# Kernel tuning notes

Measured on AMD Instinct MI355X. Metric: run time of the kernel, lower is better.

## Reference

```python
import jax, jax.numpy as jnp
import numpy as np

B, N, D = 4, 2048, 1024
H = 8
DK = D // H            # 128, head qk dim (pre feature map)
DV = D // H            # 128, head v dim
DF = 2 * DK            # 256, hedgehog feature dim
CHUNK = 64
RMS_EPS = 1e-5


def setup_inputs() -> dict:
    key = jax.random.key(0)
    ks = jax.random.split(key, 10)
    s = D ** -0.5
    x = jax.random.normal(ks[0], (B, N, D), dtype=jnp.float32)
    Wq = jax.random.normal(ks[1], (D, D), dtype=jnp.float32) * s
    Wk = jax.random.normal(ks[2], (D, D), dtype=jnp.float32) * s
    Wv = jax.random.normal(ks[3], (D, D), dtype=jnp.float32) * s
    Wo = jax.random.normal(ks[4], (D, D), dtype=jnp.float32) * s
    eye = jnp.eye(DK, dtype=jnp.float32)
    # Hedgehog maps are initialized as identity; add small noise to exercise math
    fmq_w = eye + 0.02 * jax.random.normal(ks[5], (DK, DK), dtype=jnp.float32)
    fmq_b = 0.02 * jax.random.normal(ks[6], (DK,), dtype=jnp.float32)
    fmk_w = eye + 0.02 * jax.random.normal(ks[7], (DK, DK), dtype=jnp.float32)
    fmk_b = 0.02 * jax.random.normal(ks[8], (DK,), dtype=jnp.float32)
    rms_w = 1.0 + 0.1 * jax.random.normal(ks[9], (DV,), dtype=jnp.float32)
    return {"x": x, "Wq": Wq, "Wk": Wk, "Wv": Wv, "Wo": Wo,
            "fmq_w": fmq_w, "fmq_b": fmq_b, "fmk_w": fmk_w, "fmk_b": fmk_b,
            "rms_w": rms_w}


def _hedgehog(x, w, b):
    # x: [B,H,N,DK]; Linear then concat(exp(y), exp(-y)) -> [B,H,N,2*DK]
    y = jnp.einsum('bhnd,ed->bhne', x, w) + b
    return jnp.concatenate([jnp.exp(y), jnp.exp(-y)], axis=-1)


def _fused_chunk_linear_attn(q, k, v):
    # Causal linear attention via chunked recurrence.
    # q,k: [B,H,N,DF]; v: [B,H,N,DV]; q already scaled.
    b, h, n, df = q.shape
    dv = v.shape[-1]
    nc = n // CHUNK
    def to_chunks(t):
        d = t.shape[-1]
        return t.reshape(b, h, nc, CHUNK, d).transpose(2, 0, 1, 3, 4)  # [Nc,B,H,C,d]
    qc, kc, vc = to_chunks(q), to_chunks(k), to_chunks(v)
    mask = jnp.tril(jnp.ones((CHUNK, CHUNK), dtype=bool))

    def step(S, inp):
        qi, ki, vi = inp                                   # [B,H,C,*]
        attn = jnp.einsum('bhcd,bhed->bhce', qi, ki)       # intra-chunk scores
        attn = jnp.where(mask, attn, 0.0)                  # causal (inclusive)
        intra = jnp.einsum('bhce,bhev->bhcv', attn, vi)
        inter = jnp.einsum('bhcd,bhdv->bhcv', qi, S)       # past-chunk state
        S = S + jnp.einsum('bhcd,bhcv->bhdv', ki, vi)
        return S, intra + inter

    S0 = jnp.zeros((b, h, df, dv), dtype=q.dtype)
    _, oc = jax.lax.scan(step, S0, (qc, kc, vc))           # oc: [Nc,B,H,C,DV]
    return oc.transpose(1, 2, 0, 3, 4).reshape(b, h, n, dv)


def reference(x, Wq, Wk, Wv, Wo, fmq_w, fmq_b, fmk_w, fmk_b, rms_w):
    b, n, d = x.shape
    split = lambda t: t.reshape(b, n, H, -1).transpose(0, 2, 1, 3)  # b h n d
    q = split(x @ Wq.T)
    k = split(x @ Wk.T)
    v = split(x @ Wv.T)
    q = _hedgehog(q, fmq_w, fmq_b)          # [B,H,N,DF]
    k = _hedgehog(k, fmk_w, fmk_b)
    scale = q.shape[-1] ** -0.5             # fla default: feat_dim**-0.5
    o = _fused_chunk_linear_attn(q * scale, k, v)
    # RMSNorm over head_v_dim
    o = o * jax.lax.rsqrt(jnp.mean(o * o, axis=-1, keepdims=True) + RMS_EPS) * rms_w
    o = o.transpose(0, 2, 1, 3).reshape(b, n, H * DV)
    return o @ Wo.T
```

## Files before the change

kernel.cpp:

```cpp
#include <hip/hip_runtime.h>
#include <cstdint>
#include <cstddef>

#define DEV __device__ __forceinline__

typedef __attribute__((ext_vector_type(8))) short   short8;
typedef __attribute__((ext_vector_type(4))) short   sshort4;
typedef __attribute__((ext_vector_type(8))) __bf16  bf16x8;
typedef __attribute__((ext_vector_type(4))) float   f32x4;

typedef void as1_void __attribute__((address_space(1)));
typedef void as3_void __attribute__((address_space(3)));

DEV short f2b(float f) {
  unsigned u = __float_as_uint(f);
  unsigned r = (u + 0x7fffu + ((u >> 16) & 1u)) >> 16;
  return (short)r;
}
DEV float b2f(short s) {
  return __uint_as_float(((unsigned)(unsigned short)s) << 16);
}

DEV void gload16(const void* g, void* l) {
  __builtin_amdgcn_global_load_lds((as1_void*)g, (as3_void*)l, 16, 0, 0);
}

DEV bf16x8 ld8(const short* p) { return *reinterpret_cast<const bf16x8*>(p); }

DEV f32x4 mfma16(bf16x8 a, bf16x8 b, f32x4 c) {
  return __builtin_amdgcn_mfma_f32_16x16x32_bf16(a, b, c, 0, 0, 0);
}

__global__ void convert_kernel(const float* __restrict__ src, short* __restrict__ dst, int n) {
  int i = (blockIdx.x * 256 + threadIdx.x) * 8;
  if (i + 8 > n) return;
  float4 a = *(const float4*)(src + i);
  float4 b = *(const float4*)(src + i + 4);
  short8 o;
  o[0] = f2b(a.x); o[1] = f2b(a.y); o[2] = f2b(a.z); o[3] = f2b(a.w);
  o[4] = f2b(b.x); o[5] = f2b(b.y); o[6] = f2b(b.z); o[7] = f2b(b.w);
  *(short8*)(dst + i) = o;
}

__global__ void eff_weights2_kernel(const float* __restrict__ Wq, const float* __restrict__ Wk,
                                    const float* __restrict__ fmq_w, const float* __restrict__ fmk_w,
                                    short* __restrict__ Wcat)
{
  __shared__ float fm[16 * 128];
  const int blk = blockIdx.x;
  const int sel = blk >> 6, h = (blk >> 3) & 7, eg = blk & 7;
  const float* W   = sel ? Wk : Wq;
  const float* fmw = sel ? fmk_w : fmq_w;
  const int tid = threadIdx.x;
  const int e0 = eg * 16;
  for (int i = tid; i < 2048; i += 256) fm[i] = fmw[e0 * 128 + i];
  __syncthreads();
  float acc[16][4] = {};
  for (int d = 0; d < 128; d += 4) {
    f32x4 w0 = *(const f32x4*)(W + (size_t)(h * 128 + d + 0) * 1024 + tid * 4);
    f32x4 w1 = *(const f32x4*)(W + (size_t)(h * 128 + d + 1) * 1024 + tid * 4);
    f32x4 w2 = *(const f32x4*)(W + (size_t)(h * 128 + d + 2) * 1024 + tid * 4);
    f32x4 w3 = *(const f32x4*)(W + (size_t)(h * 128 + d + 3) * 1024 + tid * 4);
#pragma unroll
    for (int e = 0; e < 16; ++e) {
      f32x4 fv = *(const f32x4*)&fm[e * 128 + d];
#pragma unroll
      for (int c = 0; c < 4; ++c)
        acc[e][c] += fv[0] * w0[c] + fv[1] * w1[c] + fv[2] * w2[c] + fv[3] * w3[c];
    }
  }
#pragma unroll
  for (int e = 0; e < 16; ++e) {
    sshort4 o;
#pragma unroll
    for (int c = 0; c < 4; ++c) o[c] = f2b(acc[e][c]);
    *(sshort4*)(Wcat + (size_t)(sel * 1024 + h * 128 + e0 + e) * 1024 + tid * 4) = o;
  }
}

template<int EPI>
__launch_bounds__(256, 3)
__global__ void gemm_bt(const short* __restrict__ A, const short* __restrict__ B,
                        int K, int N, float* __restrict__ C,
                        const float* __restrict__ qb, const float* __restrict__ kb,
                        short* __restrict__ qf, short* __restrict__ kf,
                        short* __restrict__ kfT, short* __restrict__ vT)
{
  __shared__ __align__(16) char smem[33792];
  short* lds = (short*)smem;
  float* ep  = (float*)smem;

  const int tid = threadIdx.x;
  const int w = tid >> 6, l = tid & 63;
  const int wr = w >> 1, wc = w & 1;

  const int nbx = gridDim.x;
  const int orig = blockIdx.y * nbx + blockIdx.x;
  const int cpx = (nbx * gridDim.y) >> 3;
  const int wg = (orig & 7) * cpx + (orig >> 3);
  const int m0 = (wg / nbx) * 128, n0 = (wg % nbx) * 128;

  short* ldsA = lds;
  short* ldsB = lds + 8192;
  const int sr8 = l >> 3;
  const int sl8 = ((l & 7) ^ sr8) * 8;

  f32x4 acc[4][4] = {};

  for (int k0 = 0; k0 < K; k0 += 64) {
    __syncthreads();
#pragma unroll
    for (int j = 0; j < 4; ++j) {
      const int seg = w * 4 + j;
      const int row = seg * 8 + sr8;
      gload16(A + (size_t)(m0 + row) * K + k0 + sl8, ldsA + seg * 512);
      gload16(B + (size_t)(n0 + row) * K + k0 + sl8, ldsB + seg * 512);
    }
    __syncthreads();
#pragma unroll
    for (int kk = 0; kk < 2; ++kk) {
      const int rs = ((kk * 4 + (l >> 4)) ^ (l & 7)) * 8;
      bf16x8 af[4], bfr[4];
#pragma unroll
      for (int m = 0; m < 4; ++m)
        af[m] = ld8(ldsA + (wr * 64 + m * 16 + (l & 15)) * 64 + rs);
#pragma unroll
      for (int n = 0; n < 4; ++n)
        bfr[n] = ld8(ldsB + (wc * 64 + n * 16 + (l & 15)) * 64 + rs);
#pragma unroll
      for (int m = 0; m < 4; ++m)
#pragma unroll
        for (int n = 0; n < 4; ++n)
          acc[m][n] = mfma16(af[m], bfr[n], acc[m][n]);
    }
  }

  const int seg = (EPI == 1) ? (n0 >> 10) : 0;
  const int b   = m0 >> 11, tok0 = m0 & 2047, c0 = tok0 >> 6;
  const int h   = (n0 & 1023) >> 7;
  const int bh  = b * 8 + h;

  for (int half = 0; half < 2; ++half) {
    __syncthreads();
    if (wr == half) {
#pragma unroll
      for (int n = 0; n < 4; ++n) {
        const int cl = wc * 64 + n * 16 + (l & 15);
        float bb = 0.f;
        if constexpr (EPI == 1) bb = (seg == 0) ? qb[cl] : (seg == 1) ? kb[cl] : 0.f;
#pragma unroll
        for (int m = 0; m < 4; ++m)
#pragma unroll
          for (int r = 0; r < 4; ++r) {
            const int rl = m * 16 + (l >> 4) * 4 + r;
            ep[rl * 132 + (cl ^ ((rl & 7) << 2))] = acc[m][n][r] + bb;
          }
      }
    }
    __syncthreads();

    if constexpr (EPI == 0) {
#pragma unroll
      for (int it = 0; it < 8; ++it) {
        const int tl = it * 8 + (tid >> 5);
        const int q = tid & 31;
        f32x4 v4 = *(const f32x4*)&ep[tl * 132 + ((q * 4) ^ ((tl & 7) << 2))];
        *(f32x4*)(C + (size_t)(m0 + half * 64 + tl) * N + n0 + q * 4) = v4;
      }
    } else {
      if (seg <= 1) {
        short* dst = (seg == 0) ? qf : kf;
        const float sc = (seg == 0) ? 0.0625f : 1.0f;
#pragma unroll
        for (int it = 0; it < 8; ++it) {
          const int tl = it * 8 + (tid >> 5);
          const int q = tid & 31;
          f32x4 y4 = *(const f32x4*)&ep[tl * 132 + ((q * 4) ^ ((tl & 7) << 2))];
          sshort4 sp, sm;
#pragma unroll
          for (int j = 0; j < 4; ++j) {
            sp[j] = f2b(__expf(y4[j]) * sc);
            sm[j] = f2b(__expf(-y4[j]) * sc);
          }
          short* rowp = dst + ((size_t)bh * 2048 + tok0 + half * 64 + tl) * 256;
          *(sshort4*)(rowp + q * 4)       = sp;
          *(sshort4*)(rowp + 128 + q * 4) = sm;
        }
        if (seg == 1) {
#pragma unroll
          for (int p2 = 0; p2 < 8; ++p2) {
            const int r = p2 * 32 + (tid >> 3);
            const int e = r & 127, sg = r >> 7;
            const int oct = (tid & 7) * 8;
            short8 o;
#pragma unroll
            for (int i = 0; i < 8; ++i) {
              float y = ep[(oct + i) * 132 + (e ^ (i << 2))];
              o[i] = f2b(__expf(sg ? -y : y));
            }
            *(short8*)(kfT + (((size_t)bh * 32 + c0 + half) * 256 + r) * 64 + oct) = o;
          }
        }
      } else {
#pragma unroll
        for (int p2 = 0; p2 < 4; ++p2) {
          const int r = p2 * 32 + (tid >> 3);
          const int oct = (tid & 7) * 8;
          short8 o;
#pragma unroll
          for (int i = 0; i < 8; ++i)
            o[i] = f2b(ep[(oct + i) * 132 + (r ^ (i << 2))]);
          *(short8*)(vT + (((size_t)bh * 32 + c0 + half) * 128 + r) * 64 + oct) = o;
        }
      }
    }
  }
}

__launch_bounds__(256, 3)
__global__ void passA_kernel(const short* __restrict__ kfT, const short* __restrict__ vT,
                             short* __restrict__ GT)
{
  const int bhc = blockIdx.x;
  const int tid = threadIdx.x, w = tid >> 6, l = tid & 63;
  __shared__ __align__(16) short skT[256 * 64];
  __shared__ __align__(16) short svt[128 * 64];
  const short* kg = kfT + (size_t)bhc * 256 * 64;
  const short* vg = vT  + (size_t)bhc * 128 * 64;
  short* G = GT + (size_t)bhc * 128 * 256;
  const int sr8 = l >> 3, sl8 = ((l & 7) ^ sr8) * 8;

#pragma unroll
  for (int j = 0; j < 8; ++j) {
    const int seg = w * 8 + j;
    gload16(kg + (size_t)(seg * 8 + sr8) * 64 + sl8, skT + seg * 512);
  }
#pragma unroll
  for (int j = 0; j < 4; ++j) {
    const int seg = w * 4 + j;
    gload16(vg + (size_t)(seg * 8 + sr8) * 64 + sl8, svt + seg * 512);
  }
  __syncthreads();

#pragma unroll
  for (int mi = 0; mi < 2; ++mi) {
    const int v0 = w * 32 + mi * 16;
    bf16x8 a[2];
#pragma unroll
    for (int ks = 0; ks < 2; ++ks)
      a[ks] = ld8(svt + (v0 + (l & 15)) * 64 + ((ks * 4 + (l >> 4)) ^ (l & 7)) * 8);
    f32x4 acc[16] = {};
#pragma unroll
    for (int nt = 0; nt < 16; ++nt)
#pragma unroll
      for (int ks = 0; ks < 2; ++ks) {
        bf16x8 b = ld8(skT + (nt * 16 + (l & 15)) * 64 + ((ks * 4 + (l >> 4)) ^ (l & 7)) * 8);
        acc[nt] = mfma16(a[ks], b, acc[nt]);
      }
#pragma unroll
    for (int nt = 0; nt < 16; ++nt)
#pragma unroll
      for (int r = 0; r < 4; ++r)
        G[(v0 + (l >> 4) * 4 + r) * 256 + nt * 16 + (l & 15)] = f2b(acc[nt][r]);
  }
}

__global__ void prefix_kernel(short* __restrict__ GT) {
  const int bh = blockIdx.x >> 4, slab = blockIdx.x & 15;
  short* base = GT + (size_t)bh * 32 * 32768 + slab * 2048 + threadIdx.x * 8;
  float acc[8] = {};
  short8 g = *(const short8*)base;
  for (int c = 0; c < 32; ++c) {
    short* p = base + (size_t)c * 32768;
    short8 gn = {};
    if (c < 31) gn = *(const short8*)(p + 32768);
    short8 s;
#pragma unroll
    for (int j = 0; j < 8; ++j) s[j] = f2b(acc[j]);
    *(short8*)p = s;
#pragma unroll
    for (int j = 0; j < 8; ++j) acc[j] += b2f(g[j]);
    g = gn;
  }
}

__launch_bounds__(256, 3)
__global__ void passC_kernel(const short* __restrict__ qf, const short* __restrict__ kf,
                             const short* __restrict__ vT, const short* __restrict__ ST,
                             const float* __restrict__ rms_w, short* __restrict__ o_n)
{
  const int bhc = blockIdx.x, bh = bhc >> 5, c = bhc & 31;
  const int tid = threadIdx.x, w = tid >> 6, l = tid & 63;
  __shared__ __align__(16) short bufA[64 * 256];
  __shared__ __align__(16) short bufV[64 * 64];
  __shared__ __align__(16) short attn[64 * 72];
  const short* qg = qf + ((size_t)bh * 2048 + c * 64) * 256;
  const short* kg = kf + ((size_t)bh * 2048 + c * 64) * 256;
  const short* vg = vT + (size_t)bhc * 128 * 64;
  const short* sg = ST + (size_t)bhc * 128 * 256;
  const int r0 = w * 16;
  const int sr8 = l >> 3, sl8 = ((l & 7) ^ sr8) * 8;
  const int l5 = l >> 5, s32 = l & 31;

#pragma unroll
  for (int j = 0; j < 8; ++j) {
    const int seg = w * 8 + j;
    const int row = seg * 2 + l5;
    gload16(kg + (size_t)row * 256 + (s32 ^ (row & 7)) * 8, bufA + seg * 512);
  }
  bf16x8 qreg[8];
#pragma unroll
  for (int ks = 0; ks < 8; ++ks)
    qreg[ks] = ld8(qg + (size_t)(r0 + (l & 15)) * 256 + ks * 32 + (l >> 4) * 8);

  __syncthreads();
  f32x4 s[4] = {};
#pragma unroll
  for (int ks = 0; ks < 8; ++ks) {
    const int rs = ((ks * 4 + (l >> 4)) ^ (l & 7)) * 8;
#pragma unroll
    for (int nt = 0; nt < 4; ++nt)
      s[nt] = mfma16(qreg[ks], ld8(bufA + (nt * 16 + (l & 15)) * 256 + rs), s[nt]);
  }
#pragma unroll
  for (int nt = 0; nt < 4; ++nt)
#pragma unroll
    for (int r = 0; r < 4; ++r) {
      int rr = r0 + (l >> 4) * 4 + r;
      int tt = nt * 16 + (l & 15);
      attn[rr * 72 + tt] = (tt <= rr) ? f2b(s[nt][r]) : (short)0;
    }

  f32x4 o[8] = {};
#pragma unroll
  for (int h = 0; h < 2; ++h) {
    __syncthreads();
#pragma unroll
    for (int j = 0; j < 8; ++j) {
      const int seg = w * 8 + j;
      const int row = seg * 2 + l5;
      gload16(sg + (size_t)(h * 64 + row) * 256 + (s32 ^ (row & 7)) * 8, bufA + seg * 512);
    }
#pragma unroll
    for (int j = 0; j < 2; ++j) {
      const int seg = w * 2 + j;
      const int row = seg * 8 + sr8;
      gload16(vg + (size_t)(h * 64 + row) * 64 + sl8, bufV + seg * 512);
    }
    __syncthreads();
#pragma unroll
    for (int ks = 0; ks < 2; ++ks) {
      bf16x8 a = ld8(attn + (r0 + (l & 15)) * 72 + ks * 32 + (l >> 4) * 8);
      const int rs = ((ks * 4 + (l >> 4)) ^ (l & 7)) * 8;
#pragma unroll
      for (int nt = 0; nt < 4; ++nt)
        o[h * 4 + nt] = mfma16(a, ld8(bufV + (nt * 16 + (l & 15)) * 64 + rs), o[h * 4 + nt]);
    }
#pragma unroll
    for (int ks = 0; ks < 8; ++ks) {
      const int rs = ((ks * 4 + (l >> 4)) ^ (l & 7)) * 8;
#pragma unroll
      for (int nt = 0; nt < 4; ++nt)
        o[h * 4 + nt] = mfma16(qreg[ks], ld8(bufA + (nt * 16 + (l & 15)) * 256 + rs), o[h * 4 + nt]);
    }
  }

  const int b = bh >> 3, hh = bh & 7;
#pragma unroll
  for (int r = 0; r < 4; ++r) {
    float ss = 0.f;
#pragma unroll
    for (int nt = 0; nt < 8; ++nt) ss += o[nt][r] * o[nt][r];
    ss += __shfl_xor(ss, 1);
    ss += __shfl_xor(ss, 2);
    ss += __shfl_xor(ss, 4);
    ss += __shfl_xor(ss, 8);
    float sc = rsqrtf(ss * (1.0f / 128.0f) + 1e-5f);
    int tok = c * 64 + r0 + (l >> 4) * 4 + r;
    size_t ob = ((size_t)b * 2048 + tok) * 1024 + hh * 128;
#pragma unroll
    for (int nt = 0; nt < 8; ++nt) {
      int vcol = nt * 16 + (l & 15);
      o_n[ob + vcol] = f2b(o[nt][r] * sc * rms_w[vcol]);
    }
  }
}

extern "C" void kernel_launch(void* const* d_in, const int* in_sizes, int n_in,
                              void* d_out, int out_size, void* d_ws, size_t ws_size,
                              hipStream_t stream)
{
  const float* x     = (const float*)d_in[0];
  const float* Wq    = (const float*)d_in[1];
  const float* Wk    = (const float*)d_in[2];
  const float* Wv    = (const float*)d_in[3];
  const float* Wo    = (const float*)d_in[4];
  const float* fmq_w = (const float*)d_in[5];
  const float* fmq_b = (const float*)d_in[6];
  const float* fmk_w = (const float*)d_in[7];
  const float* fmk_b = (const float*)d_in[8];
  const float* rms_w = (const float*)d_in[9];
  float* out = (float*)d_out;

  char* ws = (char*)d_ws;
  short* x_b  = (short*)(ws);
  short* Wcat = (short*)(ws + 16777216);
  short* Wo_b = (short*)(ws + 23068672);
  short* qf   = (short*)(ws + 25165824);
  short* kf   = (short*)(ws + 58720256);
  short* kfT  = (short*)(ws + 92274688);
  short* vT   = (short*)(ws + 125829120);
  short* GT   = (short*)(ws + 142606336);
  short* o_n  = x_b;

  convert_kernel<<<4096, 256, 0, stream>>>(x, x_b, 8388608);
  convert_kernel<<<512, 256, 0, stream>>>(Wo, Wo_b, 1048576);
  convert_kernel<<<512, 256, 0, stream>>>(Wv, Wcat + 2097152, 1048576);
  eff_weights2_kernel<<<128, 256, 0, stream>>>(Wq, Wk, fmq_w, fmk_w, Wcat);
  gemm_bt<1><<<dim3(24, 64), 256, 0, stream>>>(x_b, Wcat, 1024, 3072, nullptr,
                                               fmq_b, fmk_b, qf, kf, kfT, vT);
  passA_kernel<<<1024, 256, 0, stream>>>(kfT, vT, GT);
  prefix_kernel<<<512, 256, 0, stream>>>(GT);
  passC_kernel<<<1024, 256, 0, stream>>>(qf, kf, vT, GT, rms_w, o_n);
  gemm_bt<0><<<dim3(8, 64), 256, 0, stream>>>(o_n, Wo_b, 1024, 1024, out,
                                              nullptr, nullptr, nullptr, nullptr,
                                              nullptr, nullptr);
}
```

Measured before the change: 371.3 us.

## Replace 128x128 GEMM with double-buffered 256x256 tile, 8-wave pipelined kernel

Both projection GEMMs now use 256x256 output tiles with 512 threads, 128 KB of LDS and two ping-pong buffers. Global-to-LDS loads for later K steps are interleaved with the MFMA phases, with explicit waitcnt, barrier and setprio scheduling. The aim is to raise data reuse per loaded byte and hide load latency behind compute. The cost is fewer workgroups (384 and 128), which may underfill the 256 CUs, and an epilogue with more complex per-head index remapping.

```diff
diff --git a/kernel.cpp b/kernel.cpp
--- a/kernel.cpp
+++ b/kernel.cpp
@@ -79,81 +79,128 @@
 }
 
 template<int EPI>
-__launch_bounds__(256, 3)
-__global__ void gemm_bt(const short* __restrict__ A, const short* __restrict__ B,
-                        int K, int N, float* __restrict__ C,
+__launch_bounds__(512, 2)
+__global__ void gemm256(const short* __restrict__ A, const short* __restrict__ B,
+                        const int K, const int N, float* __restrict__ C,
                         const float* __restrict__ qb, const float* __restrict__ kb,
                         short* __restrict__ qf, short* __restrict__ kf,
                         short* __restrict__ kfT, short* __restrict__ vT)
 {
-  __shared__ __align__(16) char smem[33792];
-  short* lds = (short*)smem;
-  float* ep  = (float*)smem;
+  __shared__ __align__(16) short lds[65536];
+  float* ep = (float*)lds;
 
   const int tid = threadIdx.x;
   const int w = tid >> 6, l = tid & 63;
-  const int wr = w >> 1, wc = w & 1;
+  const int wr = w >> 2, wc = w & 3;
 
   const int nbx = gridDim.x;
   const int orig = blockIdx.y * nbx + blockIdx.x;
   const int cpx = (nbx * gridDim.y) >> 3;
   const int wg = (orig & 7) * cpx + (orig >> 3);
-  const int m0 = (wg / nbx) * 128, n0 = (wg % nbx) * 128;
-
-  short* ldsA = lds;
-  short* ldsB = lds + 8192;
-  const int sr8 = l >> 3;
-  const int sl8 = ((l & 7) ^ sr8) * 8;
-
-  f32x4 acc[4][4] = {};
-
-  for (int k0 = 0; k0 < K; k0 += 64) {
+  const int m0 = (wg / nbx) * 256, n0 = (wg % nbx) * 256;
+
+  const int srow = tid >> 3;
+  const int scol = ((tid & 7) ^ (srow & 7)) * 8;
+  const int wbase = w * 8;
+
+  f32x4 acc[8][4] = {};
+
+  auto STG = [&](const short* src, int g0, int p, int aoff, int R, int t) {
+    gload16(src + (size_t)(g0 + R + srow) * K + t * 64 + scol,
+            lds + p * 32768 + aoff + (R + wbase) * 64);
+  };
+
+#pragma unroll
+  for (int R = 0; R < 256; R += 64) {
+    STG(A, m0, 0, 0, R, 0);
+    STG(B, n0, 0, 16384, R, 0);
+    STG(A, m0, 1, 0, R, 1);
+    STG(B, n0, 1, 16384, R, 1);
+  }
+  asm volatile("s_waitcnt vmcnt(0)" ::: "memory");
+  __builtin_amdgcn_s_barrier();
+
+#define PHASE(p, q, STAGES, TAIL) { \
+    bf16x8 af[4][2], bf[2][2]; \
+    _Pragma("unroll") \
+    for (int m = 0; m < 4; ++m) { \
+      const int r = wr * 128 + ((q) >> 1) * 64 + m * 16 + (l & 15); \
+      _Pragma("unroll") \
+      for (int kk = 0; kk < 2; ++kk) \
+        af[m][kk] = ld8(lds + (p) * 32768 + r * 64 + ((kk * 4 + (l >> 4)) ^ (r & 7)) * 8); \
+    } \
+    _Pragma("unroll") \
+    for (int n = 0; n < 2; ++n) { \
+      const int r = wc * 64 + ((q) & 1) * 32 + n * 16 + (l & 15); \
+      _Pragma("unroll") \
+      for (int kk = 0; kk < 2; ++kk) \
+        bf[n][kk] = ld8(lds + (p) * 32768 + 16384 + r * 64 + ((kk * 4 + (l >> 4)) ^ (r & 7)) * 8); \
+    } \
+    STAGES; \
+    __builtin_amdgcn_s_barrier(); \
+    asm volatile("s_waitcnt lgkmcnt(0)" ::: "memory"); \
+    __builtin_amdgcn_sched_barrier(0); \
+    __builtin_amdgcn_s_setprio(1); \
+    _Pragma("unroll") \
+    for (int m = 0; m < 4; ++m) \
+      _Pragma("unroll") \
+      for (int n = 0; n < 2; ++n) \
+        _Pragma("unroll") \
+        for (int kk = 0; kk < 2; ++kk) \
+          acc[((q) >> 1) * 4 + m][((q) & 1) * 2 + n] = \
+            mfma16(af[m][kk], bf[n][kk], acc[((q) >> 1) * 4 + m][((q) & 1) * 2 + n]); \
+    __builtin_amdgcn_s_setprio(0); \
+    TAIL; \
+    __builtin_amdgcn_s_barrier(); \
+  }
+
+  const int NI = K >> 7;
+  for (int i = 0; i < NI; ++i) {
+    const int t1 = 2 * i + 1, t2 = 2 * i + 2, t3 = 2 * i + 3;
+    const bool sE = (i < NI - 1), sL = (i > 0);
+    PHASE(0, 0, {
+      if (sL) { STG(A, m0, 1, 0, 64, t1); STG(A, m0, 1, 0, 192, t1);
+                STG(B, n0, 1, 16384, 0, t1); STG(B, n0, 1, 16384, 64, t1); } }, {});
+    PHASE(0, 1, {
+      if (sL) { STG(B, n0, 1, 16384, 128, t1); STG(B, n0, 1, 16384, 192, t1); } }, {});
+    PHASE(0, 2, {
+      if (sE) { STG(A, m0, 0, 0, 0, t2); STG(A, m0, 0, 0, 128, t2); } }, {});
+    PHASE(0, 3, {}, {
+      if (i == NI - 1) { asm volatile("s_waitcnt vmcnt(0)" ::: "memory"); }
+      else             { asm volatile("s_waitcnt vmcnt(2)" ::: "memory"); } });
+    PHASE(1, 0, {
+      if (sE) { STG(A, m0, 0, 0, 64, t2); STG(A, m0, 0, 0, 192, t2); } }, {});
+    PHASE(1, 1, {
+      if (sE) { STG(B, n0, 0, 16384, 0, t2); STG(B, n0, 0, 16384, 64, t2); } }, {});
+    PHASE(1, 2, {
+      if (sE) { STG(B, n0, 0, 16384, 128, t2); STG(B, n0, 0, 16384, 192, t2); } }, {});
+    PHASE(1, 3, {
+      if (sE) { STG(A, m0, 1, 0, 0, t3); STG(A, m0, 1, 0, 128, t3); } }, {
+      asm volatile("s_waitcnt vmcnt(2)" ::: "memory"); });
+  }
+#undef PHASE
+
+  const int seg = (EPI == 1) ? (n0 >> 10) : 0;
+  const int b = m0 >> 11, tok0 = m0 & 2047, c0 = tok0 >> 6;
+  const int hbase = (n0 & 1023) >> 7;
+  const int bh0 = b * 8 + hbase;
+
+#pragma unroll
+  for (int h = 0; h < 4; ++h) {
     __syncthreads();
-#pragma unroll
-    for (int j = 0; j < 4; ++j) {
-      const int seg = w * 4 + j;
-      const int row = seg * 8 + sr8;
-      gload16(A + (size_t)(m0 + row) * K + k0 + sl8, ldsA + seg * 512);
-      gload16(B + (size_t)(n0 + row) * K + k0 + sl8, ldsB + seg * 512);
-    }
-    __syncthreads();
-#pragma unroll
-    for (int kk = 0; kk < 2; ++kk) {
-      const int rs = ((kk * 4 + (l >> 4)) ^ (l & 7)) * 8;
-      bf16x8 af[4], bfr[4];
-#pragma unroll
-      for (int m = 0; m < 4; ++m)
-        af[m] = ld8(ldsA + (wr * 64 + m * 16 + (l & 15)) * 64 + rs);
-#pragma unroll
-      for (int n = 0; n < 4; ++n)
-        bfr[n] = ld8(ldsB + (wc * 64 + n * 16 + (l & 15)) * 64 + rs);
-#pragma unroll
-      for (int m = 0; m < 4; ++m)
-#pragma unroll
-        for (int n = 0; n < 4; ++n)
-          acc[m][n] = mfma16(af[m], bfr[n], acc[m][n]);
-    }
-  }
-
-  const int seg = (EPI == 1) ? (n0 >> 10) : 0;
-  const int b   = m0 >> 11, tok0 = m0 & 2047, c0 = tok0 >> 6;
-  const int h   = (n0 & 1023) >> 7;
-  const int bh  = b * 8 + h;
-
-  for (int half = 0; half < 2; ++half) {
-    __syncthreads();
-    if (wr == half) {
+    if (wr == (h >> 1)) {
+      const int mbase = (h & 1) * 4;
 #pragma unroll
       for (int n = 0; n < 4; ++n) {
         const int cl = wc * 64 + n * 16 + (l & 15);
         float bb = 0.f;
-        if constexpr (EPI == 1) bb = (seg == 0) ? qb[cl] : (seg == 1) ? kb[cl] : 0.f;
-#pragma unroll
-        for (int m = 0; m < 4; ++m)
+        if constexpr (EPI == 1) bb = (seg == 0) ? qb[cl & 127] : (seg == 1) ? kb[cl & 127] : 0.f;
+#pragma unroll
+        for (int m4 = 0; m4 < 4; ++m4)
 #pragma unroll
           for (int r = 0; r < 4; ++r) {
-            const int rl = m * 16 + (l >> 4) * 4 + r;
-            ep[rl * 132 + (cl ^ ((rl & 7) << 2))] = acc[m][n][r] + bb;
+            const int rl = m4 * 16 + (l >> 4) * 4 + r;
+            ep[rl * 264 + (cl ^ ((rl & 3) << 2))] = acc[mbase + m4][n][r] + bb;
           }
       }
     }
@@ -162,55 +209,59 @@
     if constexpr (EPI == 0) {
 #pragma unroll
       for (int it = 0; it < 8; ++it) {
-        const int tl = it * 8 + (tid >> 5);
-        const int q = tid & 31;
-        f32x4 v4 = *(const f32x4*)&ep[tl * 132 + ((q * 4) ^ ((tl & 7) << 2))];
-        *(f32x4*)(C + (size_t)(m0 + half * 64 + tl) * N + n0 + q * 4) = v4;
+        const int tl = it * 8 + (tid >> 6);
+        const int cc4 = (tid & 63) * 4;
+        f32x4 v4 = *(const f32x4*)&ep[tl * 264 + (cc4 ^ ((tl & 3) << 2))];
+        *(f32x4*)(C + (size_t)(m0 + h * 64 + tl) * N + n0 + cc4) = v4;
       }
     } else {
+      const int cc = c0 + h;
       if (seg <= 1) {
         short* dst = (seg == 0) ? qf : kf;
         const float sc = (seg == 0) ? 0.0625f : 1.0f;
 #pragma unroll
         for (int it = 0; it < 8; ++it) {
-          const int tl = it * 8 + (tid >> 5);
-          const int q = tid & 31;
-          f32x4 y4 = *(const f32x4*)&ep[tl * 132 + ((q * 4) ^ ((tl & 7) << 2))];
+          const int tl = it * 8 + (tid >> 6);
+          const int cc4 = (tid & 63) * 4;
+          f32x4 y4 = *(const f32x4*)&ep[tl * 264 + (cc4 ^ ((tl & 3) << 2))];
           sshort4 sp, sm;
 #pragma unroll
           for (int j = 0; j < 4; ++j) {
             sp[j] = f2b(__expf(y4[j]) * sc);
             sm[j] = f2b(__expf(-y4[j]) * sc);
           }
-          short* rowp = dst + ((size_t)bh * 2048 + tok0 + half * 64 + tl) * 256;
-          *(sshort4*)(rowp + q * 4)       = sp;
-          *(sshort4*)(rowp + 128 + q * 4) = sm;
+          const int hh = cc4 >> 7, e = cc4 & 127;
+          short* rowp = dst + ((size_t)(bh0 + hh) * 2048 + tok0 + h * 64 + tl) * 256;
+          *(sshort4*)(rowp + e)       = sp;
+          *(sshort4*)(rowp + 128 + e) = sm;
         }
         if (seg == 1) {
 #pragma unroll
           for (int p2 = 0; p2 < 8; ++p2) {
-            const int r = p2 * 32 + (tid >> 3);
-            const int e = r & 127, sg = r >> 7;
-            const int oct = (tid & 7) * 8;
+            const int idx = p2 * 512 + tid;
+            const int er = idx >> 3, oct = (idx & 7) * 8;
+            const int hh = er >> 8, rr = er & 255, e = rr & 127, sg = rr >> 7;
+            const int cgc = hh * 128 + e;
             short8 o;
 #pragma unroll
-            for (int i = 0; i < 8; ++i) {
-              float y = ep[(oct + i) * 132 + (e ^ (i << 2))];
-              o[i] = f2b(__expf(sg ? -y : y));
+            for (int ii = 0; ii < 8; ++ii) {
+              float y = ep[(oct + ii) * 264 + (cgc ^ (((oct + ii) & 3) << 2))];
+              o[ii] = f2b(__expf(sg ? -y : y));
             }
-            *(short8*)(kfT + (((size_t)bh * 32 + c0 + half) * 256 + r) * 64 + oct) = o;
+            *(short8*)(kfT + ((size_t)(bh0 + hh) * 32 + cc) * 16384 + (size_t)rr * 64 + oct) = o;
           }
         }
       } else {
 #pragma unroll
         for (int p2 = 0; p2 < 4; ++p2) {
-          const int r = p2 * 32 + (tid >> 3);
-          const int oct = (tid & 7) * 8;
+          const int idx = p2 * 512 + tid;
+          const int er = idx >> 3, oct = (idx & 7) * 8;
+          const int hh = er >> 7, vv = er & 127;
           short8 o;
 #pragma unroll
-          for (int i = 0; i < 8; ++i)
-            o[i] = f2b(ep[(oct + i) * 132 + (r ^ (i << 2))]);
-          *(short8*)(vT + (((size_t)bh * 32 + c0 + half) * 128 + r) * 64 + oct) = o;
+          for (int ii = 0; ii < 8; ++ii)
+            o[ii] = f2b(ep[(oct + ii) * 264 + (er ^ (((oct + ii) & 3) << 2))]);
+          *(short8*)(vT + ((size_t)(bh0 + hh) * 32 + cc) * 8192 + (size_t)vv * 64 + oct) = o;
         }
       }
     }
@@ -417,12 +468,12 @@
   convert_kernel<<<512, 256, 0, stream>>>(Wo, Wo_b, 1048576);
   convert_kernel<<<512, 256, 0, stream>>>(Wv, Wcat + 2097152, 1048576);
   eff_weights2_kernel<<<128, 256, 0, stream>>>(Wq, Wk, fmq_w, fmk_w, Wcat);
-  gemm_bt<1><<<dim3(24, 64), 256, 0, stream>>>(x_b, Wcat, 1024, 3072, nullptr,
+  gemm256<1><<<dim3(12, 32), 512, 0, stream>>>(x_b, Wcat, 1024, 3072, nullptr,
                                                fmq_b, fmk_b, qf, kf, kfT, vT);
   passA_kernel<<<1024, 256, 0, stream>>>(kfT, vT, GT);
   prefix_kernel<<<512, 256, 0, stream>>>(GT);
   passC_kernel<<<1024, 256, 0, stream>>>(qf, kf, vT, GT, rms_w, o_n);
-  gemm_bt<0><<<dim3(8, 64), 256, 0, stream>>>(o_n, Wo_b, 1024, 1024, out,
+  gemm256<0><<<dim3(4, 32), 512, 0, stream>>>(o_n, Wo_b, 1024, 1024, out,
                                               nullptr, nullptr, nullptr, nullptr,
                                               nullptr, nullptr);
 }
```

Result: faster. 363.3 us (-2.2%).
